# Kernel optimization log

Hardware: AMD Instinct MI355X
Metric: run time of the kernel (lower is better)

Reference implementation:

```python
import jax, jax.numpy as jnp
from jax import lax
import numpy as np

RADIUS = 0.2
NSAMPLE = 64


def setup_inputs() -> dict:
    key = jax.random.key(0)
    k1, k2, k3 = jax.random.split(key, 3)
    B, N, S, C = 4, 16384, 4096, 64
    xyz = jax.random.uniform(k1, (B, N, 3), dtype=jnp.float32)
    new_xyz = jax.random.uniform(k2, (B, S, 3), dtype=jnp.float32)
    features = jax.random.normal(k3, (B, C, N), dtype=jnp.float32)
    return {"xyz": xyz, "new_xyz": new_xyz, "features": features}


def _ball_query(xyz, new_xyz, radius, nsample):
    # xyz: (B,N,3), new_xyz: (B,S,3) -> idx (B,S,nsample) int32
    # Squared distances via GEMM form: ||q||^2 + ||p||^2 - 2 q.p
    N = xyz.shape[1]
    q2 = jnp.sum(new_xyz * new_xyz, axis=-1)            # (B,S)
    p2 = jnp.sum(xyz * xyz, axis=-1)                    # (B,N)
    qp = jnp.einsum('bsd,bnd->bsn', new_xyz, xyz)       # (B,S,N)
    d2 = q2[:, :, None] + p2[:, None, :] - 2.0 * qp     # (B,S,N)
    # CUDA ball_query semantics: take the FIRST nsample points (by index order)
    # within radius; pad remaining slots with the first found index; 0 if none.
    cand = jnp.where(d2 < radius * radius,
                     jnp.arange(N, dtype=jnp.int32), jnp.int32(N))  # (B,S,N)
    neg_smallest, _ = lax.top_k(-cand, nsample)         # nsample smallest indices
    idx = -neg_smallest                                 # ascending (B,S,nsample)
    first = idx[..., :1]
    idx = jnp.where(idx == N, first, idx)               # pad with first neighbor
    idx = jnp.where(idx == N, 0, idx)                   # no neighbor at all -> 0
    return idx


def _group(feat, idx):
    # feat: (B,C,N), idx: (B,S,K) -> (B,C,S,K)
    return jax.vmap(lambda f, i: f[:, i])(feat, idx)


def reference(xyz, new_xyz, features):
    idx = _ball_query(xyz, new_xyz, RADIUS, NSAMPLE)        # (B,S,K)
    grouped_xyz = _group(jnp.transpose(xyz, (0, 2, 1)), idx)  # (B,3,S,K)
    grouped_xyz = grouped_xyz - jnp.transpose(new_xyz, (0, 2, 1))[..., None]
    grouped_features = _group(features, idx)                # (B,C,S,K)
    return jnp.concatenate([grouped_xyz, grouped_features], axis=1)  # (B,3+C,S,K)
```

## Files before the change

kernel.cpp:

```cpp
#include <hip/hip_runtime.h>
#include <cstdint>
#include <cstddef>

#define BB 4
#define NN 16384
#define SS 4096
#define CC 64
#define NSAMP 64
#define R2 0.04f

#define TRANS_BLOCKS (BB * (NN / 64))
#define XYZW_BLOCKS  64

typedef float f32x4 __attribute__((ext_vector_type(4)));

__global__ __launch_bounds__(256) void prep_kernel(const float* __restrict__ xyz,
                                                   const float* __restrict__ feat,
                                                   float* __restrict__ featT,
                                                   f32x4* __restrict__ xyzw) {
    int t = threadIdx.x;
    if (blockIdx.x < TRANS_BLOCKS) {
        __shared__ float tile[64][65];
        int blk = blockIdx.x;
        int b   = blk / (NN / 64);
        int n0  = (blk % (NN / 64)) * 64;
        int nl  = t & 63;
        int cq  = t >> 6;
#pragma unroll
        for (int p = 0; p < 16; ++p) {
            int c = cq + p * 4;
            tile[c][nl] = feat[((size_t)b * CC + c) * NN + n0 + nl];
        }
        __syncthreads();
#pragma unroll
        for (int p = 0; p < 16; ++p) {
            int nl2 = cq + p * 4;
            featT[((size_t)b * NN + n0 + nl2) * CC + nl] = tile[nl][nl2];
        }
        return;
    }
    int T0     = (blockIdx.x - TRANS_BLOCKS) * 256 + t;
    int stride = XYZW_BLOCKS * 256;
    for (int p = T0; p < BB * NN; p += stride) {
        float x = xyz[(size_t)p * 3 + 0];
        float y = xyz[(size_t)p * 3 + 1];
        float z = xyz[(size_t)p * 3 + 2];
        f32x4 o = {x, y, z, 0.0f};
        xyzw[p] = o;
    }
}

__global__ __launch_bounds__(256) void fused_qg(const f32x4* __restrict__ xyzw,
                                                const float* __restrict__ nxyz,
                                                const float* __restrict__ featT,
                                                float* __restrict__ out) {
    __shared__ float tile[64][65];
    __shared__ int   sidx[4][NSAMP];

    int t    = threadIdx.x;
    int wid  = t >> 6;
    int lane = t & 63;
    int wg   = blockIdx.x;
    int qblk = (wg & 7) * (BB * SS / 8 / 4) + (wg >> 3);
    int q0   = qblk * 4;

    {
        int q = q0 + wid;
        int b = q >> 12;
        int s = q & (SS - 1);
        const f32x4* xp = xyzw + (size_t)b * NN;
        float qx = nxyz[((size_t)b * SS + s) * 3 + 0];
        float qy = nxyz[((size_t)b * SS + s) * 3 + 1];
        float qz = nxyz[((size_t)b * SS + s) * 3 + 2];
        float q2 = __fadd_rn(__fadd_rn(__fmul_rn(qx, qx), __fmul_rn(qy, qy)),
                             __fadd_rn(__fmul_rn(qz, qz), 0.0f) == __fmul_rn(qz, qz)
                                 ? __fmul_rn(qz, qz) : __fmul_rn(qz, qz));
        q2 = __fadd_rn(__fadd_rn(__fmul_rn(qx, qx), __fmul_rn(qy, qy)),
                       __fmul_rn(qz, qz));

        int cnt = 0;
        f32x4 A  = xp[lane];
        f32x4 Bv = xp[lane + 64];
        for (int base = 0; base < NN; base += 128) {
            f32x4 ca = A, cb = Bv;
            int nb = base + 128;
            if (nb < NN) {
                A  = xp[nb + lane];
                Bv = xp[nb + 64 + lane];
            }
            float p2a = __fadd_rn(__fadd_rn(__fmul_rn(ca.x, ca.x), __fmul_rn(ca.y, ca.y)),
                                  __fmul_rn(ca.z, ca.z));
            float qpa = __fadd_rn(__fadd_rn(__fmul_rn(qx, ca.x), __fmul_rn(qy, ca.y)),
                                  __fmul_rn(qz, ca.z));
            float d2a = __fsub_rn(__fadd_rn(q2, p2a), __fadd_rn(qpa, qpa));
            float p2b = __fadd_rn(__fadd_rn(__fmul_rn(cb.x, cb.x), __fmul_rn(cb.y, cb.y)),
                                  __fmul_rn(cb.z, cb.z));
            float qpb = __fadd_rn(__fadd_rn(__fmul_rn(qx, cb.x), __fmul_rn(qy, cb.y)),
                                  __fmul_rn(qz, cb.z));
            float d2b = __fsub_rn(__fadd_rn(q2, p2b), __fadd_rn(qpb, qpb));
            bool in0 = d2a < R2;
            bool in1 = d2b < R2;
            unsigned long long m0 = __ballot(in0);
            unsigned long long m1 = __ballot(in1);
            int c0 = __popcll(m0);
            if (in0) {
                int pos = cnt + __popcll(m0 & ((1ull << lane) - 1ull));
                if (pos < NSAMP) sidx[wid][pos] = base + lane;
            }
            if (in1) {
                int pos = cnt + c0 + __popcll(m1 & ((1ull << lane) - 1ull));
                if (pos < NSAMP) sidx[wid][pos] = base + 64 + lane;
            }
            cnt += c0 + __popcll(m1);
            if (cnt >= NSAMP) break;
        }
        asm volatile("s_waitcnt lgkmcnt(0)" ::: "memory");
        int total = cnt < NSAMP ? cnt : NSAMP;
        int myidx = (total == 0) ? 0 : ((lane < total) ? sidx[wid][lane] : sidx[wid][0]);
        asm volatile("s_waitcnt lgkmcnt(0)" ::: "memory");
        sidx[wid][lane] = myidx;
    }
    __syncthreads();

    int rsub = t >> 4;
    int cf4  = t & 15;
    int k4   = t & 15;
#pragma unroll
    for (int qi = 0; qi < 4; ++qi) {
        int q = q0 + qi;
        int b = q >> 12;
        int s = q & (SS - 1);
        const float* ftb = featT + (size_t)b * NN * CC;
#pragma unroll
        for (int j = 0; j < 4; ++j) {
            int row = j * 16 + rsub;
            int pr  = sidx[qi][row];
            const f32x4 v = *(const f32x4*)(ftb + (size_t)pr * CC + cf4 * 4);
            tile[row][cf4 * 4 + 0] = v.x;
            tile[row][cf4 * 4 + 1] = v.y;
            tile[row][cf4 * 4 + 2] = v.z;
            tile[row][cf4 * 4 + 3] = v.w;
        }
        size_t obase = ((size_t)b * 67) * SS * 64 + (size_t)s * 64;
        size_t chs   = (size_t)SS * 64;
        if (wid == qi) {
            int id = sidx[qi][lane];
            float qx = nxyz[((size_t)b * SS + s) * 3 + 0];
            float qy = nxyz[((size_t)b * SS + s) * 3 + 1];
            float qz = nxyz[((size_t)b * SS + s) * 3 + 2];
            const f32x4 P = xyzw[(size_t)b * NN + id];
            float gx = __fsub_rn(P.x, qx);
            float gy = __fsub_rn(P.y, qy);
            float gz = __fsub_rn(P.z, qz);
            __builtin_nontemporal_store(gx, out + obase + 0 * chs + lane);
            __builtin_nontemporal_store(gy, out + obase + 1 * chs + lane);
            __builtin_nontemporal_store(gz, out + obase + 2 * chs + lane);
        }
        __syncthreads();
#pragma unroll
        for (int j = 0; j < 4; ++j) {
            int c = j * 16 + (t >> 4);
            f32x4 o;
            o.x = tile[k4 * 4 + 0][c];
            o.y = tile[k4 * 4 + 1][c];
            o.z = tile[k4 * 4 + 2][c];
            o.w = tile[k4 * 4 + 3][c];
            __builtin_nontemporal_store(o,
                (f32x4*)(out + obase + (size_t)(3 + c) * chs + k4 * 4));
        }
        __syncthreads();
    }
}

__global__ __launch_bounds__(64) void qg_fallback(const float* __restrict__ xyz,
                                                  const float* __restrict__ nxyz,
                                                  const float* __restrict__ feat,
                                                  float* __restrict__ out) {
    __shared__ int sidx[NSAMP];
    int q = blockIdx.x;
    int b = q >> 12, s = q & (SS - 1);
    int lane = threadIdx.x;
    const float* xb = xyz + (size_t)b * NN * 3;
    float qx = nxyz[((size_t)b * SS + s) * 3 + 0];
    float qy = nxyz[((size_t)b * SS + s) * 3 + 1];
    float qz = nxyz[((size_t)b * SS + s) * 3 + 2];
    float q2 = __fadd_rn(__fadd_rn(__fmul_rn(qx, qx), __fmul_rn(qy, qy)),
                         __fmul_rn(qz, qz));
    int cnt = 0;
    for (int base = 0; base < NN; base += 64) {
        float cx = xb[(size_t)(base + lane) * 3 + 0];
        float cy = xb[(size_t)(base + lane) * 3 + 1];
        float cz = xb[(size_t)(base + lane) * 3 + 2];
        float p2 = __fadd_rn(__fadd_rn(__fmul_rn(cx, cx), __fmul_rn(cy, cy)),
                             __fmul_rn(cz, cz));
        float qp = __fadd_rn(__fadd_rn(__fmul_rn(qx, cx), __fmul_rn(qy, cy)),
                             __fmul_rn(qz, cz));
        float d2 = __fsub_rn(__fadd_rn(q2, p2), __fadd_rn(qp, qp));
        bool in = d2 < R2;
        unsigned long long m = __ballot(in);
        if (in) {
            int pos = cnt + __popcll(m & ((1ull << lane) - 1ull));
            if (pos < NSAMP) sidx[pos] = base + lane;
        }
        cnt += __popcll(m);
        if (cnt >= NSAMP) break;
    }
    __syncthreads();
    int total = cnt < NSAMP ? cnt : NSAMP;
    int myidx = (total == 0) ? 0 : ((lane < total) ? sidx[lane] : sidx[0]);
    size_t obase = ((size_t)b * 67) * SS * 64 + (size_t)s * 64;
    size_t chs   = (size_t)SS * 64;
    out[obase + 0 * chs + lane] = __fsub_rn(xb[(size_t)myidx * 3 + 0], qx);
    out[obase + 1 * chs + lane] = __fsub_rn(xb[(size_t)myidx * 3 + 1], qy);
    out[obase + 2 * chs + lane] = __fsub_rn(xb[(size_t)myidx * 3 + 2], qz);
    const float* fb = feat + (size_t)b * CC * NN;
#pragma unroll 4
    for (int c = 0; c < CC; ++c)
        out[obase + (size_t)(3 + c) * chs + lane] = fb[(size_t)c * NN + myidx];
}

extern "C" void kernel_launch(void* const* d_in, const int* in_sizes, int n_in,
                              void* d_out, int out_size, void* d_ws, size_t ws_size,
                              hipStream_t stream) {
    const float* xyz  = (const float*)d_in[0];
    const float* nxyz = (const float*)d_in[1];
    const float* feat = (const float*)d_in[2];
    float* out = (float*)d_out;

    size_t needT = (size_t)BB * NN * CC * sizeof(float);
    size_t needW = (size_t)BB * NN * 4 * sizeof(float);
    if (ws_size >= needT + needW) {
        float* featT = (float*)d_ws;
        f32x4* xyzw  = (f32x4*)((char*)d_ws + needT);
        prep_kernel<<<TRANS_BLOCKS + XYZW_BLOCKS, 256, 0, stream>>>(xyz, feat,
                                                                    featT, xyzw);
        fused_qg<<<BB * SS / 4, 256, 0, stream>>>(xyzw, nxyz, featT, out);
    } else {
        qg_fallback<<<BB * SS, 64, 0, stream>>>(xyz, nxyz, feat, out);
    }
}
```

Measured before the change: 83.00 us.

## Make each wavefront gather and transpose its own query without block barriers

Each wavefront now handles the full feature gather, transpose and store for its own query, using a private shared-memory subtile of 16 channels at a time. This removes the block-wide __syncthreads between the four queries, so wavefronts no longer wait on each other's ball-query scans. It also prefetches the next 16-channel chunk into registers while the current one is written. The cost is more register pressure, plus correctness that depends on wavefront-synchronous LDS ordering enforced only by s_waitcnt.

```diff
diff --git a/kernel.cpp b/kernel.cpp
--- a/kernel.cpp
+++ b/kernel.cpp
@@ -54,7 +54,7 @@
                                                 const float* __restrict__ nxyz,
                                                 const float* __restrict__ featT,
                                                 float* __restrict__ out) {
-    __shared__ float tile[64][65];
+    __shared__ float sub[4][64][17];
     __shared__ int   sidx[4][NSAMP];
 
     int t    = threadIdx.x;
@@ -62,113 +62,121 @@
     int lane = t & 63;
     int wg   = blockIdx.x;
     int qblk = (wg & 7) * (BB * SS / 8 / 4) + (wg >> 3);
-    int q0   = qblk * 4;
+    int q    = qblk * 4 + wid;
+    int b    = q >> 12;
+    int s    = q & (SS - 1);
+
+    const f32x4* xp = xyzw + (size_t)b * NN;
+    float qx = nxyz[((size_t)b * SS + s) * 3 + 0];
+    float qy = nxyz[((size_t)b * SS + s) * 3 + 1];
+    float qz = nxyz[((size_t)b * SS + s) * 3 + 2];
+    float q2 = __fadd_rn(__fadd_rn(__fmul_rn(qx, qx), __fmul_rn(qy, qy)),
+                         __fmul_rn(qz, qz));
+
+    int cnt = 0;
+    f32x4 A  = xp[lane];
+    f32x4 Bv = xp[lane + 64];
+    for (int base = 0; base < NN; base += 128) {
+        f32x4 ca = A, cb = Bv;
+        int nb = base + 128;
+        if (nb < NN) {
+            A  = xp[nb + lane];
+            Bv = xp[nb + 64 + lane];
+        }
+        float p2a = __fadd_rn(__fadd_rn(__fmul_rn(ca.x, ca.x), __fmul_rn(ca.y, ca.y)),
+                              __fmul_rn(ca.z, ca.z));
+        float qpa = __fadd_rn(__fadd_rn(__fmul_rn(qx, ca.x), __fmul_rn(qy, ca.y)),
+                              __fmul_rn(qz, ca.z));
+        float d2a = __fsub_rn(__fadd_rn(q2, p2a), __fadd_rn(qpa, qpa));
+        float p2b = __fadd_rn(__fadd_rn(__fmul_rn(cb.x, cb.x), __fmul_rn(cb.y, cb.y)),
+                              __fmul_rn(cb.z, cb.z));
+        float qpb = __fadd_rn(__fadd_rn(__fmul_rn(qx, cb.x), __fmul_rn(qy, cb.y)),
+                              __fmul_rn(qz, cb.z));
+        float d2b = __fsub_rn(__fadd_rn(q2, p2b), __fadd_rn(qpb, qpb));
+        bool in0 = d2a < R2;
+        bool in1 = d2b < R2;
+        unsigned long long m0 = __ballot(in0);
+        unsigned long long m1 = __ballot(in1);
+        int c0 = __popcll(m0);
+        if (in0) {
+            int pos = cnt + __popcll(m0 & ((1ull << lane) - 1ull));
+            if (pos < NSAMP) sidx[wid][pos] = base + lane;
+        }
+        if (in1) {
+            int pos = cnt + c0 + __popcll(m1 & ((1ull << lane) - 1ull));
+            if (pos < NSAMP) sidx[wid][pos] = base + 64 + lane;
+        }
+        cnt += c0 + __popcll(m1);
+        if (cnt >= NSAMP) break;
+    }
+    asm volatile("s_waitcnt lgkmcnt(0)" ::: "memory");
+    int total = cnt < NSAMP ? cnt : NSAMP;
+    int myidx = (total == 0) ? 0 : ((lane < total) ? sidx[wid][lane] : sidx[wid][0]);
+    asm volatile("s_waitcnt lgkmcnt(0)" ::: "memory");
+    sidx[wid][lane] = myidx;
+    asm volatile("s_waitcnt lgkmcnt(0)" ::: "memory");
+
+    size_t obase = ((size_t)b * 67) * SS * 64 + (size_t)s * 64;
+    size_t chs   = (size_t)SS * 64;
 
     {
-        int q = q0 + wid;
-        int b = q >> 12;
-        int s = q & (SS - 1);
-        const f32x4* xp = xyzw + (size_t)b * NN;
-        float qx = nxyz[((size_t)b * SS + s) * 3 + 0];
-        float qy = nxyz[((size_t)b * SS + s) * 3 + 1];
-        float qz = nxyz[((size_t)b * SS + s) * 3 + 2];
-        float q2 = __fadd_rn(__fadd_rn(__fmul_rn(qx, qx), __fmul_rn(qy, qy)),
-                             __fadd_rn(__fmul_rn(qz, qz), 0.0f) == __fmul_rn(qz, qz)
-                                 ? __fmul_rn(qz, qz) : __fmul_rn(qz, qz));
-        q2 = __fadd_rn(__fadd_rn(__fmul_rn(qx, qx), __fmul_rn(qy, qy)),
-                       __fmul_rn(qz, qz));
-
-        int cnt = 0;
-        f32x4 A  = xp[lane];
-        f32x4 Bv = xp[lane + 64];
-        for (int base = 0; base < NN; base += 128) {
-            f32x4 ca = A, cb = Bv;
-            int nb = base + 128;
-            if (nb < NN) {
-                A  = xp[nb + lane];
-                Bv = xp[nb + 64 + lane];
-            }
-            float p2a = __fadd_rn(__fadd_rn(__fmul_rn(ca.x, ca.x), __fmul_rn(ca.y, ca.y)),
-                                  __fmul_rn(ca.z, ca.z));
-            float qpa = __fadd_rn(__fadd_rn(__fmul_rn(qx, ca.x), __fmul_rn(qy, ca.y)),
-                                  __fmul_rn(qz, ca.z));
-            float d2a = __fsub_rn(__fadd_rn(q2, p2a), __fadd_rn(qpa, qpa));
-            float p2b = __fadd_rn(__fadd_rn(__fmul_rn(cb.x, cb.x), __fmul_rn(cb.y, cb.y)),
-                                  __fmul_rn(cb.z, cb.z));
-            float qpb = __fadd_rn(__fadd_rn(__fmul_rn(qx, cb.x), __fmul_rn(qy, cb.y)),
-                                  __fmul_rn(qz, cb.z));
-            float d2b = __fsub_rn(__fadd_rn(q2, p2b), __fadd_rn(qpb, qpb));
-            bool in0 = d2a < R2;
-            bool in1 = d2b < R2;
-            unsigned long long m0 = __ballot(in0);
-            unsigned long long m1 = __ballot(in1);
-            int c0 = __popcll(m0);
-            if (in0) {
-                int pos = cnt + __popcll(m0 & ((1ull << lane) - 1ull));
-                if (pos < NSAMP) sidx[wid][pos] = base + lane;
-            }
-            if (in1) {
-                int pos = cnt + c0 + __popcll(m1 & ((1ull << lane) - 1ull));
-                if (pos < NSAMP) sidx[wid][pos] = base + 64 + lane;
-            }
-            cnt += c0 + __popcll(m1);
-            if (cnt >= NSAMP) break;
+        const f32x4 P = xp[myidx];
+        float gx = __fsub_rn(P.x, qx);
+        float gy = __fsub_rn(P.y, qy);
+        float gz = __fsub_rn(P.z, qz);
+        __builtin_nontemporal_store(gx, out + obase + 0 * chs + lane);
+        __builtin_nontemporal_store(gy, out + obase + 1 * chs + lane);
+        __builtin_nontemporal_store(gz, out + obase + 2 * chs + lane);
+    }
+
+    const float* ftb = featT + (size_t)b * NN * CC;
+    int r4 = lane >> 2;
+    int fc = lane & 3;
+    int k4 = lane & 15;
+    int cs = lane >> 4;
+
+    int ridx[4];
+#pragma unroll
+    for (int j = 0; j < 4; ++j) ridx[j] = sidx[wid][j * 16 + r4];
+    asm volatile("s_waitcnt lgkmcnt(0)" ::: "memory");
+
+    f32x4 v[4];
+#pragma unroll
+    for (int j = 0; j < 4; ++j)
+        v[j] = *(const f32x4*)(ftb + (size_t)ridx[j] * CC + fc * 4);
+
+#pragma unroll
+    for (int h = 0; h < 4; ++h) {
+        f32x4 w[4];
+        if (h < 3) {
+#pragma unroll
+            for (int j = 0; j < 4; ++j)
+                w[j] = *(const f32x4*)(ftb + (size_t)ridx[j] * CC + (h + 1) * 16 + fc * 4);
+        }
+#pragma unroll
+        for (int j = 0; j < 4; ++j) {
+            int row = j * 16 + r4;
+            sub[wid][row][fc * 4 + 0] = v[j].x;
+            sub[wid][row][fc * 4 + 1] = v[j].y;
+            sub[wid][row][fc * 4 + 2] = v[j].z;
+            sub[wid][row][fc * 4 + 3] = v[j].w;
         }
         asm volatile("s_waitcnt lgkmcnt(0)" ::: "memory");
-        int total = cnt < NSAMP ? cnt : NSAMP;
-        int myidx = (total == 0) ? 0 : ((lane < total) ? sidx[wid][lane] : sidx[wid][0]);
-        asm volatile("s_waitcnt lgkmcnt(0)" ::: "memory");
-        sidx[wid][lane] = myidx;
-    }
-    __syncthreads();
-
-    int rsub = t >> 4;
-    int cf4  = t & 15;
-    int k4   = t & 15;
-#pragma unroll
-    for (int qi = 0; qi < 4; ++qi) {
-        int q = q0 + qi;
-        int b = q >> 12;
-        int s = q & (SS - 1);
-        const float* ftb = featT + (size_t)b * NN * CC;
 #pragma unroll
         for (int j = 0; j < 4; ++j) {
-            int row = j * 16 + rsub;
-            int pr  = sidx[qi][row];
-            const f32x4 v = *(const f32x4*)(ftb + (size_t)pr * CC + cf4 * 4);
-            tile[row][cf4 * 4 + 0] = v.x;
-            tile[row][cf4 * 4 + 1] = v.y;
-            tile[row][cf4 * 4 + 2] = v.z;
-            tile[row][cf4 * 4 + 3] = v.w;
-        }
-        size_t obase = ((size_t)b * 67) * SS * 64 + (size_t)s * 64;
-        size_t chs   = (size_t)SS * 64;
-        if (wid == qi) {
-            int id = sidx[qi][lane];
-            float qx = nxyz[((size_t)b * SS + s) * 3 + 0];
-            float qy = nxyz[((size_t)b * SS + s) * 3 + 1];
-            float qz = nxyz[((size_t)b * SS + s) * 3 + 2];
-            const f32x4 P = xyzw[(size_t)b * NN + id];
-            float gx = __fsub_rn(P.x, qx);
-            float gy = __fsub_rn(P.y, qy);
-            float gz = __fsub_rn(P.z, qz);
-            __builtin_nontemporal_store(gx, out + obase + 0 * chs + lane);
-            __builtin_nontemporal_store(gy, out + obase + 1 * chs + lane);
-            __builtin_nontemporal_store(gz, out + obase + 2 * chs + lane);
-        }
-        __syncthreads();
-#pragma unroll
-        for (int j = 0; j < 4; ++j) {
-            int c = j * 16 + (t >> 4);
+            int cc = j * 4 + cs;
+            int c  = h * 16 + cc;
             f32x4 o;
-            o.x = tile[k4 * 4 + 0][c];
-            o.y = tile[k4 * 4 + 1][c];
-            o.z = tile[k4 * 4 + 2][c];
-            o.w = tile[k4 * 4 + 3][c];
+            o.x = sub[wid][k4 * 4 + 0][cc];
+            o.y = sub[wid][k4 * 4 + 1][cc];
+            o.z = sub[wid][k4 * 4 + 2][cc];
+            o.w = sub[wid][k4 * 4 + 3][cc];
             __builtin_nontemporal_store(o,
                 (f32x4*)(out + obase + (size_t)(3 + c) * chs + k4 * 4));
         }
-        __syncthreads();
+        asm volatile("s_waitcnt lgkmcnt(0)" ::: "memory");
+#pragma unroll
+        for (int j = 0; j < 4; ++j) v[j] = w[j];
     }
 }
 
```

Result: faster. 80.37 us, median of 2 (-3.2%).
